# Kernel tuning notes

Measured on AMD Instinct MI355X. Metric: run time of the kernel, lower is better.

The kernel has to match this reference:

```python
import jax, jax.numpy as jnp
import numpy as np

FP8_MAX = 448.0   # torch.finfo(float8_e4m3fn).max
BLK = 128         # block_size = [128, 128] for weights; [1, 128] for activations
E, H, I, T, TOPK = 8, 2048, 1408, 512, 2
FP8 = jnp.float8_e4m3fn


def fp8_round(x):
    """Round-trip through float8_e4m3fn (simulates .to(float8_e4m3fn))."""
    return jnp.clip(x, -FP8_MAX, FP8_MAX).astype(FP8).astype(jnp.float32)


def setup_inputs() -> dict:
    key = jax.random.key(0)
    ks = jax.random.split(key, 7)
    hidden_states = jax.random.normal(ks[0], (T, H), jnp.float32)
    top_k_index = jax.random.randint(ks[1], (T, TOPK), 0, E)
    top_k_weights = jax.random.uniform(ks[2], (T, TOPK), jnp.float32)
    # FP8 weight codes (stored as fp32 values exactly representable in e4m3fn)
    gate_up_proj = fp8_round(jax.random.normal(ks[3], (E, 2 * I, H), jnp.float32))
    gate_up_proj_scale_inv = jax.random.uniform(ks[4], (E, (2 * I) // BLK, H // BLK), jnp.float32, 1e-4, 1e-2)
    down_proj = fp8_round(jax.random.normal(ks[5], (E, H, I), jnp.float32))
    down_proj_scale_inv = jax.random.uniform(ks[6], (E, H // BLK, I // BLK), jnp.float32, 1e-4, 1e-2)
    return {
        "hidden_states": hidden_states,
        "top_k_index": top_k_index,
        "top_k_weights": top_k_weights,
        "gate_up_proj": gate_up_proj,
        "gate_up_proj_scale_inv": gate_up_proj_scale_inv,
        "down_proj": down_proj,
        "down_proj_scale_inv": down_proj_scale_inv,
    }


def dequant_weight(wq, s):
    # wq: [E, N, K] fp8 codes; s: [E, N//BLK, K//BLK] per-128x128-block scale_inv
    e, n, k = wq.shape
    wb = wq.reshape(e, n // BLK, BLK, k // BLK, BLK)
    return (wb * s[:, :, None, :, None]).reshape(e, n, k)


def quant_dequant_act(x):
    # dynamic per-(row, 128-block) fp8 activation quantization, then dequant
    shp = x.shape
    xb = x.reshape(shp[:-1] + (shp[-1] // BLK, BLK))
    amax = jnp.max(jnp.abs(xb), axis=-1, keepdims=True)
    scale = jnp.maximum(amax, 1e-12) / FP8_MAX
    q = fp8_round(xb / scale)
    return (q * scale).reshape(shp)


def reference(hidden_states, top_k_index, top_k_weights, gate_up_proj,
              gate_up_proj_scale_inv, down_proj, down_proj_scale_inv):
    w_gu = dequant_weight(gate_up_proj, gate_up_proj_scale_inv)  # [E, 2I, H]
    w_d = dequant_weight(down_proj, down_proj_scale_inv)         # [E, H, I]
    # activation quantization is per-token-block, so unrouted tokens are
    # unaffected; dense per-expert compute + combine-weight mask equals the
    # original gather/scatter loop exactly (unrouted contributions weight 0).
    x = quant_dequant_act(hidden_states)                         # [T, H]
    gate_up = jnp.einsum('th,enh->etn', x, w_gu)                 # [E, T, 2I]
    gate, up = jnp.split(gate_up, 2, axis=-1)
    h = jax.nn.silu(gate) * up                                   # [E, T, I]
    h = quant_dequant_act(h)
    down = jnp.einsum('eti,ehi->eth', h, w_d)                    # [E, T, H]
    # combine[t, e] = sum over top-k slots routing token t to expert e
    combine = jnp.sum(jax.nn.one_hot(top_k_index, E, dtype=top_k_weights.dtype)
                      * top_k_weights[..., None], axis=1)        # [T, E]
    out = jnp.einsum('eth,te->th', down, combine)
    return out.astype(hidden_states.dtype)
```

## Files before the change

### kernel.cpp

```cpp
#include <hip/hip_runtime.h>
#include <math.h>

#define NE 8
#define HD 2048
#define ID 1408
#define NT 512
#define FP8MAX 448.0f

typedef __attribute__((ext_vector_type(4))) float floatx4;

__device__ __forceinline__ floatx4 fzero4() {
    floatx4 z; z.x = 0.f; z.y = 0.f; z.z = 0.f; z.w = 0.f; return z;
}

#define OFF_OFFS  0
#define OFF_TOK   1024
#define OFF_WGT   8192
#define OFF_ENT   16384
#define OFF_XSG   32768
#define OFF_XG    131072
#define OFF_HS    (3*1024*1024)
#define OFF_HQ    (3*1024*1024 + 65536)
#define OFF_GU    (5L*1024*1024)
#define OFF_D0    (52L*1024*1024)
#define OFF_D1    (61L*1024*1024)

#define LDA 136
#define GUQ (1024L * 2816)

__global__ void route_kernel(const int* __restrict__ tki,
                             const float* __restrict__ tkw,
                             int* __restrict__ offs,
                             int* __restrict__ tok,
                             float* __restrict__ wgt,
                             int* __restrict__ ent) {
    __shared__ int cnt[NE];
    __shared__ int cur[NE];
    __shared__ int base[NE + 1];
    int tid = threadIdx.x;
    if (tid < NE) { cnt[tid] = 0; cur[tid] = 0; }
    __syncthreads();
    int e = tki[tid];
    atomicAdd(&cnt[e], 1);
    __syncthreads();
    if (tid == 0) {
        int s = 0;
        for (int i = 0; i < NE; i++) { base[i] = s; s += cnt[i]; }
        base[NE] = s;
    }
    __syncthreads();
    int pos = atomicAdd(&cur[e], 1);
    int j = base[e] + pos;
    tok[j] = tid >> 1;
    wgt[j] = tkw[tid];
    ent[tid] = j;
    if (tid <= NE) offs[tid] = base[tid];
}

__global__ void quant_x_kernel(const float* __restrict__ x,
                               const int* __restrict__ ent,
                               unsigned char* __restrict__ xg,
                               float* __restrict__ xsg) {
    int wid = (blockIdx.x * 256 + threadIdx.x) >> 6;
    int lane = threadIdx.x & 63;
    int t = wid >> 4;
    int b = wid & 15;
    const float2 v = *(const float2*)(x + (long)t * HD + b * 128 + lane * 2);
    float am = fmaxf(fabsf(v.x), fabsf(v.y));
    #pragma unroll
    for (int m = 32; m; m >>= 1) am = fmaxf(am, __shfl_xor(am, m));
    float scale = fmaxf(am, 1e-12f) / FP8MAX;
    int p = __builtin_amdgcn_cvt_pk_fp8_f32(v.x / scale, v.y / scale, 0, false);
    unsigned short pk = (unsigned short)(p & 0xffff);
    int e0 = ent[2 * t], e1 = ent[2 * t + 1];
    *(unsigned short*)(xg + (long)e0 * HD + b * 128 + lane * 2) = pk;
    *(unsigned short*)(xg + (long)e1 * HD + b * 128 + lane * 2) = pk;
    if (lane == 0) { xsg[e0 * 16 + b] = scale; xsg[e1 * 16 + b] = scale; }
}

__global__ void quant_h_kernel(const float* __restrict__ gu,
                               unsigned char* __restrict__ hq,
                               float* __restrict__ hs) {
    int wid = (blockIdx.x * 256 + threadIdx.x) >> 6;
    int lane = threadIdx.x & 63;
    int j = wid / 11;
    int b = wid - j * 11;
    long base = (long)j * 2816 + b * 128 + lane * 2;
    float gx = 0.f, gy = 0.f, ux = 0.f, uy = 0.f;
    #pragma unroll
    for (int q = 0; q < 4; q++) {
        float2 g = *(const float2*)(gu + q * GUQ + base);
        float2 u = *(const float2*)(gu + q * GUQ + base + 1408);
        gx += g.x; gy += g.y; ux += u.x; uy += u.y;
    }
    float hx = (gx / (1.0f + expf(-gx))) * ux;
    float hy = (gy / (1.0f + expf(-gy))) * uy;
    float am = fmaxf(fabsf(hx), fabsf(hy));
    #pragma unroll
    for (int m = 32; m; m >>= 1) am = fmaxf(am, __shfl_xor(am, m));
    float scale = fmaxf(am, 1e-12f) / FP8MAX;
    int p = __builtin_amdgcn_cvt_pk_fp8_f32(hx / scale, hy / scale, 0, false);
    *(unsigned short*)(hq + (long)j * ID + b * 128 + lane * 2) =
        (unsigned short)(p & 0xffff);
    if (lane == 0) hs[j * 11 + b] = scale;
}

__global__ __launch_bounds__(256, 4) void gemm1_kernel(
    const unsigned char* __restrict__ xg,
    const float* __restrict__ xsg,
    const float* __restrict__ wgu,
    const float* __restrict__ sgu,
    const int* __restrict__ offs,
    float* __restrict__ guB) {
    int e = blockIdx.z;
    int mt = blockIdx.y;
    int jb = blockIdx.x >> 2;
    int kq = blockIdx.x & 3;
    int o0 = offs[e], o1 = offs[e + 1];
    int ne = o1 - o0;
    int m0 = mt * 128;
    if (m0 >= ne) return;
    int rem = ne - m0;
    int j0 = o0 + m0;

    __shared__ __align__(16) unsigned char Asm[128 * LDA];
    __shared__ __align__(16) unsigned char Bsm[64 * LDA];
    __shared__ __align__(16) float sxa[128 * 20];

    int tid = threadIdx.x;
    {
        int r = tid >> 1, q = tid & 1;
        int j = j0 + r; if (j >= o1) j = o0;
        float4 s0 = *(const float4*)(xsg + j * 16 + q * 8);
        float4 s1 = *(const float4*)(xsg + j * 16 + q * 8 + 4);
        *(float4*)&sxa[r * 20 + q * 8] = s0;
        *(float4*)&sxa[r * 20 + q * 8 + 4] = s1;
    }

    int wave = tid >> 6;
    int lane = tid & 63;
    int lr = lane & 15;
    int lq = lane >> 4;

    int aseg = tid & 7;
    int arow0 = tid >> 3;
    const unsigned char* aBase0;
    const unsigned char* aBase1;
    const unsigned char* aBase2;
    const unsigned char* aBase3;
    {
        int j;
        j = j0 + arow0;       if (j >= o1) j = o0; aBase0 = xg + (long)j * HD + aseg * 16;
        j = j0 + 32 + arow0;  if (j >= o1) j = o0; aBase1 = xg + (long)j * HD + aseg * 16;
        j = j0 + 64 + arow0;  if (j >= o1) j = o0; aBase2 = xg + (long)j * HD + aseg * 16;
        j = j0 + 96 + arow0;  if (j >= o1) j = o0; aBase3 = xg + (long)j * HD + aseg * 16;
    }

    int bcol = tid & 31;
    int brow0 = tid >> 5;
    const float* bG = wgu + ((long)e * 2816 + jb * 32 + brow0) * HD + bcol * 4;
    const float* bU = wgu + ((long)e * 2816 + 1408 + jb * 32 + brow0) * HD + bcol * 4;
    const float* sgp = sgu + (e * 22 + (jb >> 2)) * 16;
    const float* sup = sgu + (e * 22 + 11 + (jb >> 2)) * 16;

    floatx4 facc[8];
    #pragma unroll
    for (int i = 0; i < 8; i++) facc[i] = fzero4();

    int kbS = kq * 4, kbE = kbS + 4;

    for (int kb = kbS; kb < kbE; kb++) {
        {
            uint4 a0 = *(const uint4*)(aBase0 + kb * 128);
            uint4 a1 = *(const uint4*)(aBase1 + kb * 128);
            uint4 a2 = *(const uint4*)(aBase2 + kb * 128);
            uint4 a3 = *(const uint4*)(aBase3 + kb * 128);
            float4 f0 = *(const float4*)(bG + kb * 128);
            float4 f1 = *(const float4*)(bG + kb * 128 + 8 * HD);
            float4 f2 = *(const float4*)(bG + kb * 128 + 16 * HD);
            float4 f3 = *(const float4*)(bG + kb * 128 + 24 * HD);
            float4 f4 = *(const float4*)(bU + kb * 128);
            float4 f5 = *(const float4*)(bU + kb * 128 + 8 * HD);
            float4 f6 = *(const float4*)(bU + kb * 128 + 16 * HD);
            float4 f7 = *(const float4*)(bU + kb * 128 + 24 * HD);
            *(uint4*)(&Asm[(arow0)      * LDA + aseg * 16]) = a0;
            *(uint4*)(&Asm[(arow0 + 32) * LDA + aseg * 16]) = a1;
            *(uint4*)(&Asm[(arow0 + 64) * LDA + aseg * 16]) = a2;
            *(uint4*)(&Asm[(arow0 + 96) * LDA + aseg * 16]) = a3;
            int p0 = __builtin_amdgcn_cvt_pk_fp8_f32(f0.x, f0.y, 0, false);
            p0 = __builtin_amdgcn_cvt_pk_fp8_f32(f0.z, f0.w, p0, true);
            int p1 = __builtin_amdgcn_cvt_pk_fp8_f32(f1.x, f1.y, 0, false);
            p1 = __builtin_amdgcn_cvt_pk_fp8_f32(f1.z, f1.w, p1, true);
            int p2 = __builtin_amdgcn_cvt_pk_fp8_f32(f2.x, f2.y, 0, false);
            p2 = __builtin_amdgcn_cvt_pk_fp8_f32(f2.z, f2.w, p2, true);
            int p3 = __builtin_amdgcn_cvt_pk_fp8_f32(f3.x, f3.y, 0, false);
            p3 = __builtin_amdgcn_cvt_pk_fp8_f32(f3.z, f3.w, p3, true);
            int p4 = __builtin_amdgcn_cvt_pk_fp8_f32(f4.x, f4.y, 0, false);
            p4 = __builtin_amdgcn_cvt_pk_fp8_f32(f4.z, f4.w, p4, true);
            int p5 = __builtin_amdgcn_cvt_pk_fp8_f32(f5.x, f5.y, 0, false);
            p5 = __builtin_amdgcn_cvt_pk_fp8_f32(f5.z, f5.w, p5, true);
            int p6 = __builtin_amdgcn_cvt_pk_fp8_f32(f6.x, f6.y, 0, false);
            p6 = __builtin_amdgcn_cvt_pk_fp8_f32(f6.z, f6.w, p6, true);
            int p7 = __builtin_amdgcn_cvt_pk_fp8_f32(f7.x, f7.y, 0, false);
            p7 = __builtin_amdgcn_cvt_pk_fp8_f32(f7.z, f7.w, p7, true);
            *(unsigned int*)(&Bsm[(brow0)      * LDA + bcol * 4]) = (unsigned int)p0;
            *(unsigned int*)(&Bsm[(brow0 + 8)  * LDA + bcol * 4]) = (unsigned int)p1;
            *(unsigned int*)(&Bsm[(brow0 + 16) * LDA + bcol * 4]) = (unsigned int)p2;
            *(unsigned int*)(&Bsm[(brow0 + 24) * LDA + bcol * 4]) = (unsigned int)p3;
            *(unsigned int*)(&Bsm[(brow0 + 32) * LDA + bcol * 4]) = (unsigned int)p4;
            *(unsigned int*)(&Bsm[(brow0 + 40) * LDA + bcol * 4]) = (unsigned int)p5;
            *(unsigned int*)(&Bsm[(brow0 + 48) * LDA + bcol * 4]) = (unsigned int)p6;
            *(unsigned int*)(&Bsm[(brow0 + 56) * LDA + bcol * 4]) = (unsigned int)p7;
        }
        __syncthreads();
        floatx4 cacc[8];
        #pragma unroll
        for (int i = 0; i < 8; i++) cacc[i] = fzero4();
        #pragma unroll
        for (int ks = 0; ks < 4; ks++) {
            long a[2], b[4];
            #pragma unroll
            for (int mi = 0; mi < 2; mi++)
                a[mi] = *(const long*)(&Asm[(wave * 32 + mi * 16 + lr) * LDA + ks * 32 + lq * 8]);
            #pragma unroll
            for (int ni = 0; ni < 4; ni++)
                b[ni] = *(const long*)(&Bsm[(ni * 16 + lr) * LDA + ks * 32 + lq * 8]);
            #pragma unroll
            for (int mi = 0; mi < 2; mi++)
                #pragma unroll
                for (int ni = 0; ni < 4; ni++)
                    cacc[mi * 4 + ni] = __builtin_amdgcn_mfma_f32_16x16x32_fp8_fp8(
                        a[mi], b[ni], cacc[mi * 4 + ni], 0, 0, 0);
        }
        float sg = sgp[kb];
        float su = sup[kb];
        #pragma unroll
        for (int mi = 0; mi < 2; mi++) {
            #pragma unroll
            for (int reg = 0; reg < 4; reg++) {
                float sx = sxa[(wave * 32 + mi * 16 + lq * 4 + reg) * 20 + kb];
                #pragma unroll
                for (int ni = 0; ni < 4; ni++) {
                    float sw = (ni < 2) ? sg : su;
                    facc[mi * 4 + ni][reg] += cacc[mi * 4 + ni][reg] * (sw * sx);
                }
            }
        }
        __syncthreads();
    }

    float* gu = guB + (long)kq * GUQ;
    #pragma unroll
    for (int mi = 0; mi < 2; mi++) {
        #pragma unroll
        for (int ni = 0; ni < 4; ni++) {
            #pragma unroll
            for (int reg = 0; reg < 4; reg++) {
                int r = wave * 32 + mi * 16 + lq * 4 + reg;
                if (r < rem) {
                    long base = (long)(j0 + r) * 2816;
                    long col = (ni < 2) ? (jb * 32 + ni * 16 + lr)
                                        : (1408 + jb * 32 + (ni - 2) * 16 + lr);
                    gu[base + col] = facc[mi * 4 + ni][reg];
                }
            }
        }
    }
}

__global__ __launch_bounds__(256, 5) void gemm2_kernel(
    const unsigned char* __restrict__ hq,
    const float* __restrict__ hs,
    const float* __restrict__ wd,
    const float* __restrict__ sd,
    const int* __restrict__ offs,
    float* __restrict__ d0,
    float* __restrict__ d1) {
    int e = blockIdx.z;
    int mt = blockIdx.y;
    int jb = blockIdx.x >> 1;
    int kh = blockIdx.x & 1;
    int o0 = offs[e], o1 = offs[e + 1];
    int ne = o1 - o0;
    int m0 = mt * 128;
    if (m0 >= ne) return;
    int rem = ne - m0;
    int j0 = o0 + m0;

    __shared__ __align__(16) unsigned char Asm[128 * LDA];
    __shared__ __align__(16) unsigned char Bsm[32 * LDA];
    __shared__ __align__(16) float sha[128 * 12];

    int tid = threadIdx.x;
    if (tid < 128) {
        int j = j0 + tid;
        if (j >= o1) j = o0;
        const float* s = hs + j * 11;
        #pragma unroll
        for (int k = 0; k < 11; k++) sha[tid * 12 + k] = s[k];
    }

    int wave = tid >> 6;
    int lane = tid & 63;
    int lr = lane & 15;
    int lq = lane >> 4;

    int aseg = tid & 7;
    int arow0 = tid >> 3;
    const unsigned char* aBase0;
    const unsigned char* aBase1;
    const unsigned char* aBase2;
    const unsigned char* aBase3;
    {
        int j;
        j = j0 + arow0;       if (j >= o1) j = o0; aBase0 = hq + (long)j * ID + aseg * 16;
        j = j0 + 32 + arow0;  if (j >= o1) j = o0; aBase1 = hq + (long)j * ID + aseg * 16;
        j = j0 + 64 + arow0;  if (j >= o1) j = o0; aBase2 = hq + (long)j * ID + aseg * 16;
        j = j0 + 96 + arow0;  if (j >= o1) j = o0; aBase3 = hq + (long)j * ID + aseg * 16;
    }

    int bcol = tid & 31;
    int brow0 = tid >> 5;
    const float* bB = wd + ((long)e * HD + jb * 32 + brow0) * ID + bcol * 4;
    const float* sdp = sd + (e * 16 + (jb >> 2)) * 11;

    floatx4 facc[4];
    #pragma unroll
    for (int i = 0; i < 4; i++) facc[i] = fzero4();

    int kb0 = kh ? 6 : 0, kb1 = kh ? 11 : 6;

    for (int kb = kb0; kb < kb1; kb++) {
        {
            uint4 a0 = *(const uint4*)(aBase0 + kb * 128);
            uint4 a1 = *(const uint4*)(aBase1 + kb * 128);
            uint4 a2 = *(const uint4*)(aBase2 + kb * 128);
            uint4 a3 = *(const uint4*)(aBase3 + kb * 128);
            float4 f0 = *(const float4*)(bB + kb * 128);
            float4 f1 = *(const float4*)(bB + kb * 128 + 8 * ID);
            float4 f2 = *(const float4*)(bB + kb * 128 + 16 * ID);
            float4 f3 = *(const float4*)(bB + kb * 128 + 24 * ID);
            *(uint4*)(&Asm[(arow0)      * LDA + aseg * 16]) = a0;
            *(uint4*)(&Asm[(arow0 + 32) * LDA + aseg * 16]) = a1;
            *(uint4*)(&Asm[(arow0 + 64) * LDA + aseg * 16]) = a2;
            *(uint4*)(&Asm[(arow0 + 96) * LDA + aseg * 16]) = a3;
            int p0 = __builtin_amdgcn_cvt_pk_fp8_f32(f0.x, f0.y, 0, false);
            p0 = __builtin_amdgcn_cvt_pk_fp8_f32(f0.z, f0.w, p0, true);
            int p1 = __builtin_amdgcn_cvt_pk_fp8_f32(f1.x, f1.y, 0, false);
            p1 = __builtin_amdgcn_cvt_pk_fp8_f32(f1.z, f1.w, p1, true);
            int p2 = __builtin_amdgcn_cvt_pk_fp8_f32(f2.x, f2.y, 0, false);
            p2 = __builtin_amdgcn_cvt_pk_fp8_f32(f2.z, f2.w, p2, true);
            int p3 = __builtin_amdgcn_cvt_pk_fp8_f32(f3.x, f3.y, 0, false);
            p3 = __builtin_amdgcn_cvt_pk_fp8_f32(f3.z, f3.w, p3, true);
            *(unsigned int*)(&Bsm[(brow0)      * LDA + bcol * 4]) = (unsigned int)p0;
            *(unsigned int*)(&Bsm[(brow0 + 8)  * LDA + bcol * 4]) = (unsigned int)p1;
            *(unsigned int*)(&Bsm[(brow0 + 16) * LDA + bcol * 4]) = (unsigned int)p2;
            *(unsigned int*)(&Bsm[(brow0 + 24) * LDA + bcol * 4]) = (unsigned int)p3;
        }
        __syncthreads();
        floatx4 cacc[4];
        #pragma unroll
        for (int i = 0; i < 4; i++) cacc[i] = fzero4();
        #pragma unroll
        for (int ks = 0; ks < 4; ks++) {
            long a[2], b[2];
            #pragma unroll
            for (int mi = 0; mi < 2; mi++)
                a[mi] = *(const long*)(&Asm[(wave * 32 + mi * 16 + lr) * LDA + ks * 32 + lq * 8]);
            #pragma unroll
            for (int ni = 0; ni < 2; ni++)
                b[ni] = *(const long*)(&Bsm[(ni * 16 + lr) * LDA + ks * 32 + lq * 8]);
            #pragma unroll
            for (int mi = 0; mi < 2; mi++)
                #pragma unroll
                for (int ni = 0; ni < 2; ni++)
                    cacc[mi * 2 + ni] = __builtin_amdgcn_mfma_f32_16x16x32_fp8_fp8(
                        a[mi], b[ni], cacc[mi * 2 + ni], 0, 0, 0);
        }
        float sw = sdp[kb];
        #pragma unroll
        for (int mi = 0; mi < 2; mi++) {
            #pragma unroll
            for (int reg = 0; reg < 4; reg++) {
                float sh = sha[(wave * 32 + mi * 16 + lq * 4 + reg) * 12 + kb];
                #pragma unroll
                for (int ni = 0; ni < 2; ni++)
                    facc[mi * 2 + ni][reg] += cacc[mi * 2 + ni][reg] * (sw * sh);
            }
        }
        __syncthreads();
    }

    float* dp = kh ? d1 : d0;
    #pragma unroll
    for (int mi = 0; mi < 2; mi++) {
        #pragma unroll
        for (int ni = 0; ni < 2; ni++) {
            #pragma unroll
            for (int reg = 0; reg < 4; reg++) {
                int r = wave * 32 + mi * 16 + lq * 4 + reg;
                if (r < rem) {
                    dp[(long)(j0 + r) * HD + jb * 32 + ni * 16 + lr] =
                        facc[mi * 2 + ni][reg];
                }
            }
        }
    }
}

__global__ void combine_kernel(const float* __restrict__ d0,
                               const float* __restrict__ d1,
                               const int* __restrict__ ent,
                               const float* __restrict__ tkw,
                               float* __restrict__ out) {
    int gid = blockIdx.x * 256 + threadIdx.x;
    int t = gid >> 9;
    int c4 = gid & 511;
    int j0 = ent[2 * t], j1 = ent[2 * t + 1];
    float w0 = tkw[2 * t], w1 = tkw[2 * t + 1];
    long b0 = (long)j0 * HD + c4 * 4;
    long b1 = (long)j1 * HD + c4 * 4;
    float4 a0 = *(const float4*)(d0 + b0);
    float4 a1 = *(const float4*)(d1 + b0);
    float4 a2 = *(const float4*)(d0 + b1);
    float4 a3 = *(const float4*)(d1 + b1);
    float4 r;
    r.x = w0 * (a0.x + a1.x) + w1 * (a2.x + a3.x);
    r.y = w0 * (a0.y + a1.y) + w1 * (a2.y + a3.y);
    r.z = w0 * (a0.z + a1.z) + w1 * (a2.z + a3.z);
    r.w = w0 * (a0.w + a1.w) + w1 * (a2.w + a3.w);
    *(float4*)(out + (long)t * HD + c4 * 4) = r;
}

extern "C" void kernel_launch(void* const* d_in, const int* in_sizes, int n_in,
                              void* d_out, int out_size, void* d_ws, size_t ws_size,
                              hipStream_t stream) {
    (void)in_sizes; (void)n_in; (void)out_size; (void)ws_size;
    const float* x   = (const float*)d_in[0];
    const int*   tki = (const int*)d_in[1];
    const float* tkw = (const float*)d_in[2];
    const float* wgu = (const float*)d_in[3];
    const float* sgu = (const float*)d_in[4];
    const float* wd  = (const float*)d_in[5];
    const float* sd  = (const float*)d_in[6];
    float* out = (float*)d_out;
    char* ws = (char*)d_ws;

    int*   offs = (int*)(ws + OFF_OFFS);
    int*   tok  = (int*)(ws + OFF_TOK);
    float* wgt  = (float*)(ws + OFF_WGT);
    int*   ent  = (int*)(ws + OFF_ENT);
    float* xsg  = (float*)(ws + OFF_XSG);
    unsigned char* xg = (unsigned char*)(ws + OFF_XG);
    float* hs   = (float*)(ws + OFF_HS);
    unsigned char* hq = (unsigned char*)(ws + OFF_HQ);
    float* guB  = (float*)(ws + OFF_GU);
    float* dp0  = (float*)(ws + OFF_D0);
    float* dp1  = (float*)(ws + OFF_D1);

    route_kernel<<<1, 1024, 0, stream>>>(tki, tkw, offs, tok, wgt, ent);
    quant_x_kernel<<<2048, 256, 0, stream>>>(x, ent, xg, xsg);
    gemm1_kernel<<<dim3(176, 3, NE), 256, 0, stream>>>(xg, xsg, wgu, sgu, offs, guB);
    quant_h_kernel<<<2816, 256, 0, stream>>>(guB, hq, hs);
    gemm2_kernel<<<dim3(128, 3, NE), 256, 0, stream>>>(hq, hs, wd, sd, offs, dp0, dp1);
    combine_kernel<<<1024, 256, 0, stream>>>(dp0, dp1, ent, tkw, out);
}
```

Measured before the change: 418.6 us.

## Split gemm2 K four ways, drop LDS scale staging, raise occupancy bounds

```diff
diff --git a/kernel.cpp b/kernel.cpp
--- a/kernel.cpp
+++ b/kernel.cpp
@@ -22,11 +22,11 @@
 #define OFF_HS    (3*1024*1024)
 #define OFF_HQ    (3*1024*1024 + 65536)
 #define OFF_GU    (5L*1024*1024)
-#define OFF_D0    (52L*1024*1024)
-#define OFF_D1    (61L*1024*1024)
+#define OFF_D     (52L*1024*1024)
 
 #define LDA 136
 #define GUQ (1024L * 2816)
+#define DQ  (1024L * 2048)
 
 __global__ void route_kernel(const int* __restrict__ tki,
                              const float* __restrict__ tkw,
@@ -105,7 +105,7 @@
     if (lane == 0) hs[j * 11 + b] = scale;
 }
 
-__global__ __launch_bounds__(256, 4) void gemm1_kernel(
+__global__ __launch_bounds__(256, 6) void gemm1_kernel(
     const unsigned char* __restrict__ xg,
     const float* __restrict__ xsg,
     const float* __restrict__ wgu,
@@ -125,18 +125,8 @@
 
     __shared__ __align__(16) unsigned char Asm[128 * LDA];
     __shared__ __align__(16) unsigned char Bsm[64 * LDA];
-    __shared__ __align__(16) float sxa[128 * 20];
 
     int tid = threadIdx.x;
-    {
-        int r = tid >> 1, q = tid & 1;
-        int j = j0 + r; if (j >= o1) j = o0;
-        float4 s0 = *(const float4*)(xsg + j * 16 + q * 8);
-        float4 s1 = *(const float4*)(xsg + j * 16 + q * 8 + 4);
-        *(float4*)&sxa[r * 20 + q * 8] = s0;
-        *(float4*)&sxa[r * 20 + q * 8 + 4] = s1;
-    }
-
     int wave = tid >> 6;
     int lane = tid & 63;
     int lr = lane & 15;
@@ -162,6 +152,8 @@
     const float* bU = wgu + ((long)e * 2816 + 1408 + jb * 32 + brow0) * HD + bcol * 4;
     const float* sgp = sgu + (e * 22 + (jb >> 2)) * 16;
     const float* sup = sgu + (e * 22 + 11 + (jb >> 2)) * 16;
+
+    int srow0 = j0 + wave * 32 + lq * 4;
 
     floatx4 facc[8];
     #pragma unroll
@@ -238,7 +230,7 @@
         for (int mi = 0; mi < 2; mi++) {
             #pragma unroll
             for (int reg = 0; reg < 4; reg++) {
-                float sx = sxa[(wave * 32 + mi * 16 + lq * 4 + reg) * 20 + kb];
+                float sx = xsg[(srow0 + mi * 16 + reg) * 16 + kb];
                 #pragma unroll
                 for (int ni = 0; ni < 4; ni++) {
                     float sw = (ni < 2) ? sg : su;
@@ -268,18 +260,17 @@
     }
 }
 
-__global__ __launch_bounds__(256, 5) void gemm2_kernel(
+__global__ __launch_bounds__(256, 7) void gemm2_kernel(
     const unsigned char* __restrict__ hq,
     const float* __restrict__ hs,
     const float* __restrict__ wd,
     const float* __restrict__ sd,
     const int* __restrict__ offs,
-    float* __restrict__ d0,
-    float* __restrict__ d1) {
+    float* __restrict__ dB) {
     int e = blockIdx.z;
     int mt = blockIdx.y;
-    int jb = blockIdx.x >> 1;
-    int kh = blockIdx.x & 1;
+    int jb = blockIdx.x >> 2;
+    int kq = blockIdx.x & 3;
     int o0 = offs[e], o1 = offs[e + 1];
     int ne = o1 - o0;
     int m0 = mt * 128;
@@ -289,17 +280,8 @@
 
     __shared__ __align__(16) unsigned char Asm[128 * LDA];
     __shared__ __align__(16) unsigned char Bsm[32 * LDA];
-    __shared__ __align__(16) float sha[128 * 12];
 
     int tid = threadIdx.x;
-    if (tid < 128) {
-        int j = j0 + tid;
-        if (j >= o1) j = o0;
-        const float* s = hs + j * 11;
-        #pragma unroll
-        for (int k = 0; k < 11; k++) sha[tid * 12 + k] = s[k];
-    }
-
     int wave = tid >> 6;
     int lane = tid & 63;
     int lr = lane & 15;
@@ -324,11 +306,14 @@
     const float* bB = wd + ((long)e * HD + jb * 32 + brow0) * ID + bcol * 4;
     const float* sdp = sd + (e * 16 + (jb >> 2)) * 11;
 
+    int srow0 = j0 + wave * 32 + lq * 4;
+
     floatx4 facc[4];
     #pragma unroll
     for (int i = 0; i < 4; i++) facc[i] = fzero4();
 
-    int kb0 = kh ? 6 : 0, kb1 = kh ? 11 : 6;
+    int kb0 = (kq < 3) ? kq * 3 : 9;
+    int kb1 = (kq < 3) ? kq * 3 + 3 : 11;
 
     for (int kb = kb0; kb < kb1; kb++) {
         {
@@ -382,7 +367,7 @@
         for (int mi = 0; mi < 2; mi++) {
             #pragma unroll
             for (int reg = 0; reg < 4; reg++) {
-                float sh = sha[(wave * 32 + mi * 16 + lq * 4 + reg) * 12 + kb];
+                float sh = hs[(srow0 + mi * 16 + reg) * 11 + kb];
                 #pragma unroll
                 for (int ni = 0; ni < 2; ni++)
                     facc[mi * 2 + ni][reg] += cacc[mi * 2 + ni][reg] * (sw * sh);
@@ -391,7 +376,7 @@
         __syncthreads();
     }
 
-    float* dp = kh ? d1 : d0;
+    float* dp = dB + (long)kq * DQ;
     #pragma unroll
     for (int mi = 0; mi < 2; mi++) {
         #pragma unroll
@@ -408,8 +393,7 @@
     }
 }
 
-__global__ void combine_kernel(const float* __restrict__ d0,
-                               const float* __restrict__ d1,
+__global__ void combine_kernel(const float* __restrict__ dB,
                                const int* __restrict__ ent,
                                const float* __restrict__ tkw,
                                float* __restrict__ out) {
@@ -420,15 +404,20 @@
     float w0 = tkw[2 * t], w1 = tkw[2 * t + 1];
     long b0 = (long)j0 * HD + c4 * 4;
     long b1 = (long)j1 * HD + c4 * 4;
-    float4 a0 = *(const float4*)(d0 + b0);
-    float4 a1 = *(const float4*)(d1 + b0);
-    float4 a2 = *(const float4*)(d0 + b1);
-    float4 a3 = *(const float4*)(d1 + b1);
+    float4 s0 = {0.f, 0.f, 0.f, 0.f};
+    float4 s1 = {0.f, 0.f, 0.f, 0.f};
+    #pragma unroll
+    for (int q = 0; q < 4; q++) {
+        float4 a = *(const float4*)(dB + q * DQ + b0);
+        float4 b = *(const float4*)(dB + q * DQ + b1);
+        s0.x += a.x; s0.y += a.y; s0.z += a.z; s0.w += a.w;
+        s1.x += b.x; s1.y += b.y; s1.z += b.z; s1.w += b.w;
+    }
     float4 r;
-    r.x = w0 * (a0.x + a1.x) + w1 * (a2.x + a3.x);
-    r.y = w0 * (a0.y + a1.y) + w1 * (a2.y + a3.y);
-    r.z = w0 * (a0.z + a1.z) + w1 * (a2.z + a3.z);
-    r.w = w0 * (a0.w + a1.w) + w1 * (a2.w + a3.w);
+    r.x = w0 * s0.x + w1 * s1.x;
+    r.y = w0 * s0.y + w1 * s1.y;
+    r.z = w0 * s0.z + w1 * s1.z;
+    r.w = w0 * s0.w + w1 * s1.w;
     *(float4*)(out + (long)t * HD + c4 * 4) = r;
 }
 
@@ -455,13 +444,12 @@
     float* hs   = (float*)(ws + OFF_HS);
     unsigned char* hq = (unsigned char*)(ws + OFF_HQ);
     float* guB  = (float*)(ws + OFF_GU);
-    float* dp0  = (float*)(ws + OFF_D0);
-    float* dp1  = (float*)(ws + OFF_D1);
+    float* dB   = (float*)(ws + OFF_D);
 
     route_kernel<<<1, 1024, 0, stream>>>(tki, tkw, offs, tok, wgt, ent);
     quant_x_kernel<<<2048, 256, 0, stream>>>(x, ent, xg, xsg);
     gemm1_kernel<<<dim3(176, 3, NE), 256, 0, stream>>>(xg, xsg, wgu, sgu, offs, guB);
     quant_h_kernel<<<2816, 256, 0, stream>>>(guB, hq, hs);
-    gemm2_kernel<<<dim3(128, 3, NE), 256, 0, stream>>>(hq, hs, wd, sd, offs, dp0, dp1);
-    combine_kernel<<<1024, 256, 0, stream>>>(dp0, dp1, ent, tkw, out);
-}
+    gemm2_kernel<<<dim3(256, 3, NE), 256, 0, stream>>>(hq, hs, wd, sd, offs, dB);
+    combine_kernel<<<1024, 256, 0, stream>>>(dB, ent, tkw, out);
+}
```

Result: slower. 563.3 us (+34.6%).
